# Kernel optimization log

Hardware: AMD Instinct MI355X
Metric: run time of the kernel (lower is better)

Reference implementation:

```python
import jax, jax.numpy as jnp
import numpy as np

B = 2048
LATENT = 32
FRAME = 256
COND = 1
HIDDEN = 256
FUT = 1
E = 8
GATE_H = 64
IN_SIZE = LATENT + FRAME * COND      # 288
INTER = LATENT + HIDDEN              # 288 (must equal IN_SIZE, see forward)
OUT_SIZE = FUT * FRAME               # 256


def setup_inputs() -> dict:
    key = jax.random.key(0)
    ks = jax.random.split(key, 16)

    def kaiming(k, shape, fan_in):
        bound = np.sqrt(6.0 / fan_in).astype(np.float32)
        return jax.random.uniform(k, shape, jnp.float32, -bound, bound)

    z = jax.random.normal(ks[0], (B, IN_SIZE), jnp.float32)
    # gate MLP: Linear(IN_SIZE,64) -> ELU -> Linear(64,64) -> ELU -> Linear(64,E)
    g0_w = kaiming(ks[1], (IN_SIZE, GATE_H), IN_SIZE)
    g0_b = jnp.zeros((GATE_H,), jnp.float32)
    g1_w = kaiming(ks[2], (GATE_H, GATE_H), GATE_H)
    g1_b = jnp.zeros((GATE_H,), jnp.float32)
    g2_w = kaiming(ks[3], (GATE_H, E), GATE_H)
    g2_b = jnp.zeros((E,), jnp.float32)
    # expert layers (kaiming_uniform over [E, in, out]; bias filled with 0.01)
    w0 = kaiming(ks[4], (E, IN_SIZE, HIDDEN), IN_SIZE)
    b0 = jnp.full((E, HIDDEN), 0.01, jnp.float32)
    w1 = kaiming(ks[5], (E, INTER, HIDDEN), INTER)
    b1 = jnp.full((E, HIDDEN), 0.01, jnp.float32)
    w2 = kaiming(ks[6], (E, INTER, OUT_SIZE), INTER)
    b2 = jnp.full((E, OUT_SIZE), 0.01, jnp.float32)
    return dict(z=z, g0_w=g0_w, g0_b=g0_b, g1_w=g1_w, g1_b=g1_b,
                g2_w=g2_w, g2_b=g2_b, w0=w0, b0=b0, w1=w1, b1=b1, w2=w2, b2=b2)


def reference(z, g0_w, g0_b, g1_w, g1_b, g2_w, g2_b, w0, b0, w1, b1, w2, b2):
    # gating network -> softmax coefficients [B, E]
    h = jax.nn.elu(z @ g0_w + g0_b)
    h = jax.nn.elu(h @ g1_w + g1_b)
    coefficients = jax.nn.softmax(h @ g2_w + g2_b, axis=1)

    layers = [(w0, b0, True), (w1, b1, True), (w2, b2, False)]
    layer_out = None
    for weight, bias, has_act in layers:
        # materialize per-sample mixed weights (matches torch.matmul(coef, flat_weight).view(...))
        mixed_weight = jnp.einsum('be,eio->bio', coefficients, weight)  # [B, in, out]
        mixed_bias = coefficients @ bias                                 # [B, out]
        # baddbmm with z as [B,1,in]: per-sample vec-mat product
        out = jnp.einsum('bi,bio->bo', z, mixed_weight) + mixed_bias
        layer_out = jax.nn.elu(out) if has_act else out
    return layer_out
```

## Files before the change

### kernel.cpp

```cpp
#include <hip/hip_runtime.h>
#include <hip/hip_bf16.h>

#define B_TOTAL 2048
#define IN_SZ   288
#define GH      64
#define E_NUM   8
#define OUT_N   256
#define NKT     9

#define W2T_BLKS 576
#define ZF_BLKS  32
#define GWF_BLKS 4
#define GWF_FRAGS 46

typedef __attribute__((ext_vector_type(8))) short bf16x8;
typedef __attribute__((ext_vector_type(4))) float f32x4;

__device__ __forceinline__ float elu_f(float x) {
    return x > 0.0f ? x : (expf(x) - 1.0f);
}
__device__ __forceinline__ ushort f2bf(float f) {
    __hip_bfloat16 h = __float2bfloat16(f);
    return *reinterpret_cast<ushort*>(&h);
}

__global__ __launch_bounds__(256) void prep_kernel(
    const float* __restrict__ w2, const float* __restrict__ z,
    const float* __restrict__ g0_w, const float* __restrict__ g1_w,
    const float* __restrict__ g2_w,
    ushort* __restrict__ w2f, ushort* __restrict__ zf, ushort* __restrict__ gwf)
{
    __shared__ float ts[32][36];
    const int t = threadIdx.x;
    const int wid = t >> 6, l = t & 63;
    const int fr = l & 15, fg = l >> 4;

    if (blockIdx.x < W2T_BLKS) {
        const int e  = blockIdx.x / 72;
        const int r_ = blockIdx.x - e * 72;
        const int kt = r_ >> 3;
        const int og = r_ & 7;
        const int o0 = og * 32;
        const float* src = w2 + ((size_t)e * IN_SZ + kt * 32) * OUT_N + o0;
        {
            int r = t >> 3, c4 = t & 7;
            *(float4*)&ts[r][c4 * 4] = *(const float4*)(src + (size_t)r * OUT_N + c4 * 4);
        }
        __syncthreads();
        {
            const int fl   = t >> 7;
            const int half = (t >> 6) & 1;
            const int ll   = t & 63;
            const int qfr = ll & 15, qfg = ll >> 4;
            const int nt = og * 2 + fl;
            ushort4 u;
            u.x = f2bf(ts[qfg * 8 + half * 4 + 0][fl * 16 + qfr]);
            u.y = f2bf(ts[qfg * 8 + half * 4 + 1][fl * 16 + qfr]);
            u.z = f2bf(ts[qfg * 8 + half * 4 + 2][fl * 16 + qfr]);
            u.w = f2bf(ts[qfg * 8 + half * 4 + 3][fl * 16 + qfr]);
            size_t off = ((size_t)((e * 16 + nt) * NKT + kt)) * 512 + ll * 8 + half * 4;
            *(ushort4*)&w2f[off] = u;
        }
        return;
    }

    if (blockIdx.x < W2T_BLKS + ZF_BLKS) {
        const int mt = (blockIdx.x - W2T_BLKS) * 4 + wid;
        const int m0 = mt * 16;
        const float* zr = z + (size_t)(m0 + fr) * IN_SZ + fg * 8;
        #pragma unroll
        for (int kt = 0; kt < NKT; ++kt) {
            float4 v0 = *(const float4*)(zr + kt * 32);
            float4 v1 = *(const float4*)(zr + kt * 32 + 4);
            ushort4 u0, u1;
            u0.x = f2bf(v0.x); u0.y = f2bf(v0.y); u0.z = f2bf(v0.z); u0.w = f2bf(v0.w);
            u1.x = f2bf(v1.x); u1.y = f2bf(v1.y); u1.z = f2bf(v1.z); u1.w = f2bf(v1.w);
            size_t off = ((size_t)(mt * NKT + kt)) * 512 + l * 8;
            *(ushort4*)&zf[off]     = u0;
            *(ushort4*)&zf[off + 4] = u1;
        }
        return;
    }

    const int base = (blockIdx.x - W2T_BLKS - ZF_BLKS) * 4 + wid;
    for (int fid = base; fid < GWF_FRAGS; fid += 16) {
        float vals[8];
        if (fid < 36) {
            int nt = fid / NKT, kt = fid - nt * NKT;
            #pragma unroll
            for (int j = 0; j < 8; ++j) {
                int k = kt * 32 + fg * 8 + j;
                vals[j] = g0_w[k * GH + nt * 16 + fr];
            }
        } else if (fid < 44) {
            int q = fid - 36, nt = q >> 1, kk = q & 1;
            #pragma unroll
            for (int j = 0; j < 8; ++j) {
                int k = kk * 32 + fg * 8 + j;
                vals[j] = g1_w[k * GH + nt * 16 + fr];
            }
        } else {
            int kk = fid - 44;
            #pragma unroll
            for (int j = 0; j < 8; ++j) {
                int k = kk * 32 + fg * 8 + j;
                vals[j] = (fr < E_NUM) ? g2_w[k * E_NUM + fr] : 0.0f;
            }
        }
        ushort4 u0, u1;
        u0.x = f2bf(vals[0]); u0.y = f2bf(vals[1]); u0.z = f2bf(vals[2]); u0.w = f2bf(vals[3]);
        u1.x = f2bf(vals[4]); u1.y = f2bf(vals[5]); u1.z = f2bf(vals[6]); u1.w = f2bf(vals[7]);
        size_t off = (size_t)fid * 512 + l * 8;
        *(ushort4*)&gwf[off]     = u0;
        *(ushort4*)&gwf[off + 4] = u1;
    }
}

__global__ __launch_bounds__(128) void fused_kernel(
    const ushort* __restrict__ zf, const ushort* __restrict__ w2f,
    const ushort* __restrict__ gwf,
    const float* __restrict__ g0_b, const float* __restrict__ g1_b,
    const float* __restrict__ g2_b, const float* __restrict__ b2,
    float* __restrict__ out)
{
    __shared__ ushort hscr[2][16][72];
    __shared__ float  lgs[2][16][8];
    __shared__ float  cfsT[2][E_NUM][16];

    const int t = threadIdx.x, wv = t >> 6, l = t & 63;
    const int fr = l & 15, fg = l >> 4, fk = fg * 8;
    const int mt = blockIdx.x * 2 + wv, m0 = mt * 16;
    const int nt = blockIdx.y, n0 = nt * 16;

    bf16x8 A[9];
    #pragma unroll
    for (int kt = 0; kt < NKT; ++kt)
        A[kt] = *(const bf16x8*)(zf + ((size_t)(mt * NKT + kt)) * 512 + l * 8);

    #pragma unroll
    for (int ng = 0; ng < 4; ++ng) {
        f32x4 g = {0.f, 0.f, 0.f, 0.f};
        #pragma unroll
        for (int kt = 0; kt < NKT; ++kt) {
            bf16x8 b = *(const bf16x8*)(gwf + ((size_t)(ng * NKT + kt)) * 512 + l * 8);
            g = __builtin_amdgcn_mfma_f32_16x16x32_bf16(A[kt], b, g, 0, 0, 0);
        }
        float bias = g0_b[ng * 16 + fr];
        #pragma unroll
        for (int j = 0; j < 4; ++j)
            hscr[wv][fg * 4 + j][ng * 16 + fr] = f2bf(elu_f(g[j] + bias));
    }
    __syncthreads();

    {
        bf16x8 hA[2];
        #pragma unroll
        for (int kk = 0; kk < 2; ++kk)
            hA[kk] = *(const bf16x8*)&hscr[wv][fr][kk * 32 + fk];
        f32x4 gacc[4];
        #pragma unroll
        for (int ng = 0; ng < 4; ++ng) {
            f32x4 g = {0.f, 0.f, 0.f, 0.f};
            #pragma unroll
            for (int kk = 0; kk < 2; ++kk) {
                bf16x8 b = *(const bf16x8*)(gwf + ((size_t)(36 + ng * 2 + kk)) * 512 + l * 8);
                g = __builtin_amdgcn_mfma_f32_16x16x32_bf16(hA[kk], b, g, 0, 0, 0);
            }
            gacc[ng] = g;
        }
        __syncthreads();
        #pragma unroll
        for (int ng = 0; ng < 4; ++ng) {
            float bias = g1_b[ng * 16 + fr];
            #pragma unroll
            for (int j = 0; j < 4; ++j)
                hscr[wv][fg * 4 + j][ng * 16 + fr] = f2bf(elu_f(gacc[ng][j] + bias));
        }
    }
    __syncthreads();

    {
        bf16x8 hA[2];
        #pragma unroll
        for (int kk = 0; kk < 2; ++kk)
            hA[kk] = *(const bf16x8*)&hscr[wv][fr][kk * 32 + fk];
        f32x4 g = {0.f, 0.f, 0.f, 0.f};
        #pragma unroll
        for (int kk = 0; kk < 2; ++kk) {
            bf16x8 b = *(const bf16x8*)(gwf + ((size_t)(44 + kk)) * 512 + l * 8);
            g = __builtin_amdgcn_mfma_f32_16x16x32_bf16(hA[kk], b, g, 0, 0, 0);
        }
        if (fr < E_NUM) {
            float bias = g2_b[fr];
            #pragma unroll
            for (int j = 0; j < 4; ++j)
                lgs[wv][fg * 4 + j][fr] = g[j] + bias;
        }
    }
    __syncthreads();

    if (l < 16) {
        float m = lgs[wv][l][0];
        #pragma unroll
        for (int k = 1; k < E_NUM; ++k) m = fmaxf(m, lgs[wv][l][k]);
        float s = 0.f;
        float ex[E_NUM];
        #pragma unroll
        for (int k = 0; k < E_NUM; ++k) { ex[k] = expf(lgs[wv][l][k] - m); s += ex[k]; }
        float inv = 1.0f / s;
        #pragma unroll
        for (int k = 0; k < E_NUM; ++k) cfsT[wv][k][l] = ex[k] * inv;
    }
    __syncthreads();

    const ushort* Bp = w2f + (size_t)nt * NKT * 512 + l * 8;

    f32x4 acc = {0.f, 0.f, 0.f, 0.f};
    bf16x8 B[9];
    #pragma unroll
    for (int kt = 0; kt < NKT; ++kt)
        B[kt] = *(const bf16x8*)(Bp + (size_t)kt * 512);

    #pragma unroll
    for (int e = 0; e < E_NUM; ++e) {
        bf16x8 Bn[9];
        if (e < E_NUM - 1) {
            #pragma unroll
            for (int kt = 0; kt < NKT; ++kt)
                Bn[kt] = *(const bf16x8*)(Bp + ((size_t)((e + 1) * 16 * NKT) + kt) * 512);
        }
        f32x4 p0 = {0.f, 0.f, 0.f, 0.f};
        f32x4 p1 = {0.f, 0.f, 0.f, 0.f};
        p0 = __builtin_amdgcn_mfma_f32_16x16x32_bf16(A[0], B[0], p0, 0, 0, 0);
        p1 = __builtin_amdgcn_mfma_f32_16x16x32_bf16(A[1], B[1], p1, 0, 0, 0);
        p0 = __builtin_amdgcn_mfma_f32_16x16x32_bf16(A[2], B[2], p0, 0, 0, 0);
        p1 = __builtin_amdgcn_mfma_f32_16x16x32_bf16(A[3], B[3], p1, 0, 0, 0);
        p0 = __builtin_amdgcn_mfma_f32_16x16x32_bf16(A[4], B[4], p0, 0, 0, 0);
        p1 = __builtin_amdgcn_mfma_f32_16x16x32_bf16(A[5], B[5], p1, 0, 0, 0);
        p0 = __builtin_amdgcn_mfma_f32_16x16x32_bf16(A[6], B[6], p0, 0, 0, 0);
        p1 = __builtin_amdgcn_mfma_f32_16x16x32_bf16(A[7], B[7], p1, 0, 0, 0);
        p0 = __builtin_amdgcn_mfma_f32_16x16x32_bf16(A[8], B[8], p0, 0, 0, 0);

        float4 cv = *(const float4*)&cfsT[wv][e][fg * 4];
        float bv  = b2[e * OUT_N + n0 + fr];
        float ca[4] = {cv.x, cv.y, cv.z, cv.w};
        #pragma unroll
        for (int j = 0; j < 4; ++j)
            acc[j] = fmaf(ca[j], p0[j] + p1[j] + bv, acc[j]);

        #pragma unroll
        for (int kt = 0; kt < NKT; ++kt) B[kt] = Bn[kt];
    }

    #pragma unroll
    for (int j = 0; j < 4; ++j)
        out[(size_t)(m0 + fg * 4 + j) * OUT_N + n0 + fr] = acc[j];
}

__global__ __launch_bounds__(64) void gate_fb_kernel(
    const float* __restrict__ z,
    const float* __restrict__ g0_w, const float* __restrict__ g0_b,
    const float* __restrict__ g1_w, const float* __restrict__ g1_b,
    const float* __restrict__ g2_w, const float* __restrict__ g2_b,
    float* __restrict__ coef)
{
    __shared__ float z_s[IN_SZ];
    __shared__ float h0_s[GH];
    __shared__ float h1_s[GH];
    const int b = blockIdx.x;
    const int t = threadIdx.x;
    const float* zr = z + (size_t)b * IN_SZ;
    for (int i = t; i < IN_SZ; i += 64) z_s[i] = zr[i];
    __syncthreads();
    float a0 = g0_b[t];
    for (int i = 0; i < IN_SZ; ++i) a0 = fmaf(z_s[i], g0_w[i * GH + t], a0);
    h0_s[t] = elu_f(a0);
    __syncthreads();
    float a1 = g1_b[t];
    for (int k = 0; k < GH; ++k) a1 = fmaf(h0_s[k], g1_w[k * GH + t], a1);
    h1_s[t] = elu_f(a1);
    __syncthreads();
    if (t < E_NUM) {
        float lg = g2_b[t];
        for (int k = 0; k < GH; ++k) lg = fmaf(h1_s[k], g2_w[k * E_NUM + t], lg);
        float m = lg;
        for (int d = 1; d < 8; d <<= 1) m = fmaxf(m, __shfl_xor(m, d, 8));
        float ex = expf(lg - m);
        float s = ex;
        for (int d = 1; d < 8; d <<= 1) s += __shfl_xor(s, d, 8);
        coef[b * E_NUM + t] = ex / s;
    }
}

__global__ __launch_bounds__(256) void direct_kernel(
    const float* __restrict__ z, const float* __restrict__ w2,
    const float* __restrict__ b2, const float* __restrict__ coef,
    float* __restrict__ out)
{
    __shared__ float z_s[8][IN_SZ];
    __shared__ float c_s[8][E_NUM];
    const int b0 = blockIdx.x * 8;
    const int t  = threadIdx.x;
    for (int idx = t; idx < 8 * IN_SZ; idx += 256)
        ((float*)z_s)[idx] = z[(size_t)b0 * IN_SZ + idx];
    if (t < 64) c_s[t >> 3][t & 7] = coef[b0 * E_NUM + t];
    __syncthreads();
    float outv[8];
    #pragma unroll
    for (int r = 0; r < 8; ++r) outv[r] = 0.0f;
    for (int e = 0; e < E_NUM; ++e) {
        const float* w = w2 + (size_t)e * IN_SZ * OUT_N + t;
        float tmp[8];
        #pragma unroll
        for (int r = 0; r < 8; ++r) tmp[r] = 0.0f;
        #pragma unroll 4
        for (int i = 0; i < IN_SZ; ++i) {
            float wv = w[i * OUT_N];
            #pragma unroll
            for (int r = 0; r < 8; ++r) tmp[r] += z_s[r][i] * wv;
        }
        float bv = b2[e * OUT_N + t];
        #pragma unroll
        for (int r = 0; r < 8; ++r) outv[r] += c_s[r][e] * (tmp[r] + bv);
    }
    #pragma unroll
    for (int r = 0; r < 8; ++r) out[(size_t)(b0 + r) * OUT_N + t] = outv[r];
}

extern "C" void kernel_launch(void* const* d_in, const int* in_sizes, int n_in,
                              void* d_out, int out_size, void* d_ws, size_t ws_size,
                              hipStream_t stream) {
    const float* z    = (const float*)d_in[0];
    const float* g0_w = (const float*)d_in[1];
    const float* g0_b = (const float*)d_in[2];
    const float* g1_w = (const float*)d_in[3];
    const float* g1_b = (const float*)d_in[4];
    const float* g2_w = (const float*)d_in[5];
    const float* g2_b = (const float*)d_in[6];
    const float* w2   = (const float*)d_in[11];
    const float* b2   = (const float*)d_in[12];
    float* out = (float*)d_out;

    const size_t w2f_b = (size_t)E_NUM * 16 * NKT * 1024;
    const size_t zf_b  = (size_t)128 * NKT * 1024;
    const size_t gwf_b = (size_t)GWF_FRAGS * 1024;

    char* p = (char*)d_ws;
    ushort* w2f = (ushort*)p;            p += w2f_b;
    ushort* zf  = (ushort*)p;            p += zf_b;
    ushort* gwf = (ushort*)p;

    if (ws_size >= w2f_b + zf_b + gwf_b) {
        prep_kernel<<<W2T_BLKS + ZF_BLKS + GWF_BLKS, 256, 0, stream>>>(
            w2, z, g0_w, g1_w, g2_w, w2f, zf, gwf);
        fused_kernel<<<dim3(B_TOTAL / 32, OUT_N / 16), 128, 0, stream>>>(
            zf, w2f, gwf, g0_b, g1_b, g2_b, b2, out);
    } else {
        float* coef = (float*)d_ws;
        gate_fb_kernel<<<B_TOTAL, 64, 0, stream>>>(z, g0_w, g0_b, g1_w, g1_b,
                                                   g2_w, g2_b, coef);
        direct_kernel<<<B_TOTAL / 8, 256, 0, stream>>>(z, w2, b2, coef, out);
    }
}
```

Measured before the change: 22.91 us.

## Share expert weight tiles across four waves via double-buffered LDS staging

Blocks grow from 2 to 4 waves (64 rows each), and the per-expert w2 fragments are loaded cooperatively into a double-buffered LDS tile, two experts at a time, instead of each wave streaming its own copy from global memory. Register prefetch of the next expert pair overlaps the global loads with the MFMA work. This cuts redundant global/L2 traffic for weights, at the cost of extra LDS use, block-wide barriers, and half as many blocks in the grid.

```diff
diff --git a/kernel.cpp b/kernel.cpp
--- a/kernel.cpp
+++ b/kernel.cpp
@@ -116,26 +116,39 @@
     }
 }
 
-__global__ __launch_bounds__(128) void fused_kernel(
+__global__ __launch_bounds__(256) void fused_kernel(
     const ushort* __restrict__ zf, const ushort* __restrict__ w2f,
     const ushort* __restrict__ gwf,
     const float* __restrict__ g0_b, const float* __restrict__ g1_b,
     const float* __restrict__ g2_b, const float* __restrict__ b2,
     float* __restrict__ out)
 {
-    __shared__ ushort hscr[2][16][72];
-    __shared__ float  lgs[2][16][8];
-    __shared__ float  cfsT[2][E_NUM][16];
+    __shared__ ushort Bl[2][18 * 512];
+    __shared__ ushort hscr[4][16][72];
+    __shared__ float  lgs[4][16][8];
+    __shared__ float  cfsT[4][E_NUM][16];
 
     const int t = threadIdx.x, wv = t >> 6, l = t & 63;
     const int fr = l & 15, fg = l >> 4, fk = fg * 8;
-    const int mt = blockIdx.x * 2 + wv, m0 = mt * 16;
+    const int mt = blockIdx.x * 4 + wv, m0 = mt * 16;
     const int nt = blockIdx.y, n0 = nt * 16;
 
     bf16x8 A[9];
     #pragma unroll
     for (int kt = 0; kt < NKT; ++kt)
         A[kt] = *(const bf16x8*)(zf + ((size_t)(mt * NKT + kt)) * 512 + l * 8);
+
+    const int4* w2f_i4 = (const int4*)w2f;
+    int4 st[5];
+    #pragma unroll
+    for (int it = 0; it < 5; ++it) {
+        int s = t + it * 256;
+        if (s < 1152) {
+            int f = s >> 6, ll = s & 63;
+            int el = (f >= 9) ? 1 : 0, ktf = f - 9 * el;
+            st[it] = w2f_i4[((size_t)((el * 16 + nt) * NKT + ktf)) * 64 + ll];
+        }
+    }
 
     #pragma unroll
     for (int ng = 0; ng < 4; ++ng) {
@@ -213,43 +226,49 @@
     }
     __syncthreads();
 
-    const ushort* Bp = w2f + (size_t)nt * NKT * 512 + l * 8;
-
     f32x4 acc = {0.f, 0.f, 0.f, 0.f};
-    bf16x8 B[9];
-    #pragma unroll
-    for (int kt = 0; kt < NKT; ++kt)
-        B[kt] = *(const bf16x8*)(Bp + (size_t)kt * 512);
-
-    #pragma unroll
-    for (int e = 0; e < E_NUM; ++e) {
-        bf16x8 Bn[9];
-        if (e < E_NUM - 1) {
-            #pragma unroll
-            for (int kt = 0; kt < NKT; ++kt)
-                Bn[kt] = *(const bf16x8*)(Bp + ((size_t)((e + 1) * 16 * NKT) + kt) * 512);
-        }
-        f32x4 p0 = {0.f, 0.f, 0.f, 0.f};
-        f32x4 p1 = {0.f, 0.f, 0.f, 0.f};
-        p0 = __builtin_amdgcn_mfma_f32_16x16x32_bf16(A[0], B[0], p0, 0, 0, 0);
-        p1 = __builtin_amdgcn_mfma_f32_16x16x32_bf16(A[1], B[1], p1, 0, 0, 0);
-        p0 = __builtin_amdgcn_mfma_f32_16x16x32_bf16(A[2], B[2], p0, 0, 0, 0);
-        p1 = __builtin_amdgcn_mfma_f32_16x16x32_bf16(A[3], B[3], p1, 0, 0, 0);
-        p0 = __builtin_amdgcn_mfma_f32_16x16x32_bf16(A[4], B[4], p0, 0, 0, 0);
-        p1 = __builtin_amdgcn_mfma_f32_16x16x32_bf16(A[5], B[5], p1, 0, 0, 0);
-        p0 = __builtin_amdgcn_mfma_f32_16x16x32_bf16(A[6], B[6], p0, 0, 0, 0);
-        p1 = __builtin_amdgcn_mfma_f32_16x16x32_bf16(A[7], B[7], p1, 0, 0, 0);
-        p0 = __builtin_amdgcn_mfma_f32_16x16x32_bf16(A[8], B[8], p0, 0, 0, 0);
-
-        float4 cv = *(const float4*)&cfsT[wv][e][fg * 4];
-        float bv  = b2[e * OUT_N + n0 + fr];
-        float ca[4] = {cv.x, cv.y, cv.z, cv.w};
-        #pragma unroll
-        for (int j = 0; j < 4; ++j)
-            acc[j] = fmaf(ca[j], p0[j] + p1[j] + bv, acc[j]);
-
-        #pragma unroll
-        for (int kt = 0; kt < NKT; ++kt) B[kt] = Bn[kt];
+
+    #pragma unroll
+    for (int ep = 0; ep < 4; ++ep) {
+        const int buf = ep & 1;
+        #pragma unroll
+        for (int it = 0; it < 5; ++it) {
+            int s = t + it * 256;
+            if (s < 1152) ((int4*)&Bl[buf][0])[s] = st[it];
+        }
+        __syncthreads();
+        if (ep < 3) {
+            #pragma unroll
+            for (int it = 0; it < 5; ++it) {
+                int s = t + it * 256;
+                if (s < 1152) {
+                    int f = s >> 6, ll = s & 63;
+                    int el = (f >= 9) ? 1 : 0, ktf = f - 9 * el;
+                    int e = (ep + 1) * 2 + el;
+                    st[it] = w2f_i4[((size_t)((e * 16 + nt) * NKT + ktf)) * 64 + ll];
+                }
+            }
+        }
+        #pragma unroll
+        for (int el = 0; el < 2; ++el) {
+            const int e = ep * 2 + el;
+            const ushort* bp = &Bl[buf][el * 9 * 512] + l * 8;
+            f32x4 p0 = {0.f, 0.f, 0.f, 0.f};
+            f32x4 p1 = {0.f, 0.f, 0.f, 0.f};
+            #pragma unroll
+            for (int kt = 0; kt < NKT; ++kt) {
+                bf16x8 b = *(const bf16x8*)(bp + kt * 512);
+                if (kt & 1) p1 = __builtin_amdgcn_mfma_f32_16x16x32_bf16(A[kt], b, p1, 0, 0, 0);
+                else        p0 = __builtin_amdgcn_mfma_f32_16x16x32_bf16(A[kt], b, p0, 0, 0, 0);
+            }
+            float4 cv = *(const float4*)&cfsT[wv][e][fg * 4];
+            float bv  = b2[e * OUT_N + n0 + fr];
+            float ca[4] = {cv.x, cv.y, cv.z, cv.w};
+            #pragma unroll
+            for (int j = 0; j < 4; ++j)
+                acc[j] = fmaf(ca[j], p0[j] + p1[j] + bv, acc[j]);
+        }
+        __syncthreads();
     }
 
     #pragma unroll
@@ -353,7 +372,7 @@
     if (ws_size >= w2f_b + zf_b + gwf_b) {
         prep_kernel<<<W2T_BLKS + ZF_BLKS + GWF_BLKS, 256, 0, stream>>>(
             w2, z, g0_w, g1_w, g2_w, w2f, zf, gwf);
-        fused_kernel<<<dim3(B_TOTAL / 32, OUT_N / 16), 128, 0, stream>>>(
+        fused_kernel<<<dim3(B_TOTAL / 64, OUT_N / 16), 256, 0, stream>>>(
             zf, w2f, gwf, g0_b, g1_b, g2_b, b2, out);
     } else {
         float* coef = (float*)d_ws;
```

After: 31.57 us. 37.8% more time.

## Share gate MLP across four output-tile waves per row tile

Applied to the files above, without the earlier changes.

Restructures the fused kernel so each 256-thread block handles one 16-row tile and four 16-column output tiles, one per wave. The gate MLP layers are split across the four waves, each computing 16 of the 64 hidden units, and the results are shared through LDS. Before, every block of 128 threads recomputed the full gate network for its rows at each column tile, so the gating work was duplicated 16 times per row. The change cuts that duplication to 4 times, at the cost of more barriers and one wave doing the final logits alone.

```diff
diff --git a/kernel.cpp b/kernel.cpp
--- a/kernel.cpp
+++ b/kernel.cpp
@@ -116,39 +116,38 @@
     }
 }
 
-__global__ __launch_bounds__(128) void fused_kernel(
+__global__ __launch_bounds__(256) void fused_kernel(
     const ushort* __restrict__ zf, const ushort* __restrict__ w2f,
     const ushort* __restrict__ gwf,
     const float* __restrict__ g0_b, const float* __restrict__ g1_b,
     const float* __restrict__ g2_b, const float* __restrict__ b2,
     float* __restrict__ out)
 {
-    __shared__ ushort hscr[2][16][72];
-    __shared__ float  lgs[2][16][8];
-    __shared__ float  cfsT[2][E_NUM][16];
+    __shared__ ushort hscr[16][72];
+    __shared__ float  lgs[16][8];
+    __shared__ float  cfsT[E_NUM][16];
 
     const int t = threadIdx.x, wv = t >> 6, l = t & 63;
     const int fr = l & 15, fg = l >> 4, fk = fg * 8;
-    const int mt = blockIdx.x * 2 + wv, m0 = mt * 16;
-    const int nt = blockIdx.y, n0 = nt * 16;
+    const int mt = blockIdx.x, m0 = mt * 16;
+    const int nt = blockIdx.y * 4 + wv, n0 = nt * 16;
 
     bf16x8 A[9];
     #pragma unroll
     for (int kt = 0; kt < NKT; ++kt)
         A[kt] = *(const bf16x8*)(zf + ((size_t)(mt * NKT + kt)) * 512 + l * 8);
 
-    #pragma unroll
-    for (int ng = 0; ng < 4; ++ng) {
+    {
         f32x4 g = {0.f, 0.f, 0.f, 0.f};
         #pragma unroll
         for (int kt = 0; kt < NKT; ++kt) {
-            bf16x8 b = *(const bf16x8*)(gwf + ((size_t)(ng * NKT + kt)) * 512 + l * 8);
+            bf16x8 b = *(const bf16x8*)(gwf + ((size_t)(wv * NKT + kt)) * 512 + l * 8);
             g = __builtin_amdgcn_mfma_f32_16x16x32_bf16(A[kt], b, g, 0, 0, 0);
         }
-        float bias = g0_b[ng * 16 + fr];
+        float bias = g0_b[wv * 16 + fr];
         #pragma unroll
         for (int j = 0; j < 4; ++j)
-            hscr[wv][fg * 4 + j][ng * 16 + fr] = f2bf(elu_f(g[j] + bias));
+            hscr[fg * 4 + j][wv * 16 + fr] = f2bf(elu_f(g[j] + bias));
     }
     __syncthreads();
 
@@ -156,34 +155,26 @@
         bf16x8 hA[2];
         #pragma unroll
         for (int kk = 0; kk < 2; ++kk)
-            hA[kk] = *(const bf16x8*)&hscr[wv][fr][kk * 32 + fk];
-        f32x4 gacc[4];
-        #pragma unroll
-        for (int ng = 0; ng < 4; ++ng) {
-            f32x4 g = {0.f, 0.f, 0.f, 0.f};
-            #pragma unroll
-            for (int kk = 0; kk < 2; ++kk) {
-                bf16x8 b = *(const bf16x8*)(gwf + ((size_t)(36 + ng * 2 + kk)) * 512 + l * 8);
-                g = __builtin_amdgcn_mfma_f32_16x16x32_bf16(hA[kk], b, g, 0, 0, 0);
-            }
-            gacc[ng] = g;
+            hA[kk] = *(const bf16x8*)&hscr[fr][kk * 32 + fk];
+        f32x4 g = {0.f, 0.f, 0.f, 0.f};
+        #pragma unroll
+        for (int kk = 0; kk < 2; ++kk) {
+            bf16x8 b = *(const bf16x8*)(gwf + ((size_t)(36 + wv * 2 + kk)) * 512 + l * 8);
+            g = __builtin_amdgcn_mfma_f32_16x16x32_bf16(hA[kk], b, g, 0, 0, 0);
         }
         __syncthreads();
-        #pragma unroll
-        for (int ng = 0; ng < 4; ++ng) {
-            float bias = g1_b[ng * 16 + fr];
-            #pragma unroll
-            for (int j = 0; j < 4; ++j)
-                hscr[wv][fg * 4 + j][ng * 16 + fr] = f2bf(elu_f(gacc[ng][j] + bias));
-        }
-    }
-    __syncthreads();
-
-    {
+        float bias = g1_b[wv * 16 + fr];
+        #pragma unroll
+        for (int j = 0; j < 4; ++j)
+            hscr[fg * 4 + j][wv * 16 + fr] = f2bf(elu_f(g[j] + bias));
+    }
+    __syncthreads();
+
+    if (wv == 0) {
         bf16x8 hA[2];
         #pragma unroll
         for (int kk = 0; kk < 2; ++kk)
-            hA[kk] = *(const bf16x8*)&hscr[wv][fr][kk * 32 + fk];
+            hA[kk] = *(const bf16x8*)&hscr[fr][kk * 32 + fk];
         f32x4 g = {0.f, 0.f, 0.f, 0.f};
         #pragma unroll
         for (int kk = 0; kk < 2; ++kk) {
@@ -194,22 +185,22 @@
             float bias = g2_b[fr];
             #pragma unroll
             for (int j = 0; j < 4; ++j)
-                lgs[wv][fg * 4 + j][fr] = g[j] + bias;
-        }
-    }
-    __syncthreads();
-
-    if (l < 16) {
-        float m = lgs[wv][l][0];
-        #pragma unroll
-        for (int k = 1; k < E_NUM; ++k) m = fmaxf(m, lgs[wv][l][k]);
+                lgs[fg * 4 + j][fr] = g[j] + bias;
+        }
+    }
+    __syncthreads();
+
+    if (t < 16) {
+        float m = lgs[t][0];
+        #pragma unroll
+        for (int k = 1; k < E_NUM; ++k) m = fmaxf(m, lgs[t][k]);
         float s = 0.f;
         float ex[E_NUM];
         #pragma unroll
-        for (int k = 0; k < E_NUM; ++k) { ex[k] = expf(lgs[wv][l][k] - m); s += ex[k]; }
+        for (int k = 0; k < E_NUM; ++k) { ex[k] = expf(lgs[t][k] - m); s += ex[k]; }
         float inv = 1.0f / s;
         #pragma unroll
-        for (int k = 0; k < E_NUM; ++k) cfsT[wv][k][l] = ex[k] * inv;
+        for (int k = 0; k < E_NUM; ++k) cfsT[k][t] = ex[k] * inv;
     }
     __syncthreads();
 
@@ -241,7 +232,7 @@
         p1 = __builtin_amdgcn_mfma_f32_16x16x32_bf16(A[7], B[7], p1, 0, 0, 0);
         p0 = __builtin_amdgcn_mfma_f32_16x16x32_bf16(A[8], B[8], p0, 0, 0, 0);
 
-        float4 cv = *(const float4*)&cfsT[wv][e][fg * 4];
+        float4 cv = *(const float4*)&cfsT[e][fg * 4];
         float bv  = b2[e * OUT_N + n0 + fr];
         float ca[4] = {cv.x, cv.y, cv.z, cv.w};
         #pragma unroll
@@ -353,7 +344,7 @@
     if (ws_size >= w2f_b + zf_b + gwf_b) {
         prep_kernel<<<W2T_BLKS + ZF_BLKS + GWF_BLKS, 256, 0, stream>>>(
             w2, z, g0_w, g1_w, g2_w, w2f, zf, gwf);
-        fused_kernel<<<dim3(B_TOTAL / 32, OUT_N / 16), 128, 0, stream>>>(
+        fused_kernel<<<dim3(B_TOTAL / 16, OUT_N / 64), 256, 0, stream>>>(
             zf, w2f, gwf, g0_b, g1_b, g2_b, b2, out);
     } else {
         float* coef = (float*)d_ws;
```

After: 21.08 us. -8.0%, faster.

## Prefetch expert weights before gating, drop block barriers, use 4-wave blocks

Applied to the files above, without the earlier changes.

Moves the first expert's weight fragment loads and all bias loads ahead of the gating MLP so their latency overlaps the gate MFMAs. It removes every __syncthreads, since each wave only touches its own shared-memory slice. It replaces the register copy of the next expert's weights with a ping-pong pair of buffers. Blocks grow from 2 to 4 waves, halving the block count. The cost is higher register pressure from the extra live buffers, and the LDS exchange within a wave now has no explicit barrier or fence.

```diff
diff --git a/kernel.cpp b/kernel.cpp
--- a/kernel.cpp
+++ b/kernel.cpp
@@ -116,26 +116,36 @@
     }
 }
 
-__global__ __launch_bounds__(128) void fused_kernel(
+__global__ __launch_bounds__(256) void fused_kernel(
     const ushort* __restrict__ zf, const ushort* __restrict__ w2f,
     const ushort* __restrict__ gwf,
     const float* __restrict__ g0_b, const float* __restrict__ g1_b,
     const float* __restrict__ g2_b, const float* __restrict__ b2,
     float* __restrict__ out)
 {
-    __shared__ ushort hscr[2][16][72];
-    __shared__ float  lgs[2][16][8];
-    __shared__ float  cfsT[2][E_NUM][16];
+    __shared__ ushort hscr[4][16][72];
+    __shared__ float  lgs[4][16][8];
+    __shared__ float  cfsT[4][E_NUM][16];
 
     const int t = threadIdx.x, wv = t >> 6, l = t & 63;
     const int fr = l & 15, fg = l >> 4, fk = fg * 8;
-    const int mt = blockIdx.x * 2 + wv, m0 = mt * 16;
+    const int mt = blockIdx.x * 4 + wv, m0 = mt * 16;
     const int nt = blockIdx.y, n0 = nt * 16;
 
     bf16x8 A[9];
     #pragma unroll
     for (int kt = 0; kt < NKT; ++kt)
         A[kt] = *(const bf16x8*)(zf + ((size_t)(mt * NKT + kt)) * 512 + l * 8);
+
+    const ushort* Bp = w2f + (size_t)nt * NKT * 512 + l * 8;
+    bf16x8 Bb0[9], Bb1[9];
+    #pragma unroll
+    for (int kt = 0; kt < NKT; ++kt)
+        Bb0[kt] = *(const bf16x8*)(Bp + (size_t)kt * 512);
+    float bvv[E_NUM];
+    #pragma unroll
+    for (int e = 0; e < E_NUM; ++e)
+        bvv[e] = b2[e * OUT_N + n0 + fr];
 
     #pragma unroll
     for (int ng = 0; ng < 4; ++ng) {
@@ -150,7 +160,6 @@
         for (int j = 0; j < 4; ++j)
             hscr[wv][fg * 4 + j][ng * 16 + fr] = f2bf(elu_f(g[j] + bias));
     }
-    __syncthreads();
 
     {
         bf16x8 hA[2];
@@ -168,7 +177,6 @@
             }
             gacc[ng] = g;
         }
-        __syncthreads();
         #pragma unroll
         for (int ng = 0; ng < 4; ++ng) {
             float bias = g1_b[ng * 16 + fr];
@@ -177,7 +185,6 @@
                 hscr[wv][fg * 4 + j][ng * 16 + fr] = f2bf(elu_f(gacc[ng][j] + bias));
         }
     }
-    __syncthreads();
 
     {
         bf16x8 hA[2];
@@ -197,7 +204,6 @@
                 lgs[wv][fg * 4 + j][fr] = g[j] + bias;
         }
     }
-    __syncthreads();
 
     if (l < 16) {
         float m = lgs[wv][l][0];
@@ -211,45 +217,31 @@
         #pragma unroll
         for (int k = 0; k < E_NUM; ++k) cfsT[wv][k][l] = ex[k] * inv;
     }
-    __syncthreads();
-
-    const ushort* Bp = w2f + (size_t)nt * NKT * 512 + l * 8;
 
     f32x4 acc = {0.f, 0.f, 0.f, 0.f};
-    bf16x8 B[9];
-    #pragma unroll
-    for (int kt = 0; kt < NKT; ++kt)
-        B[kt] = *(const bf16x8*)(Bp + (size_t)kt * 512);
 
     #pragma unroll
     for (int e = 0; e < E_NUM; ++e) {
-        bf16x8 Bn[9];
         if (e < E_NUM - 1) {
             #pragma unroll
-            for (int kt = 0; kt < NKT; ++kt)
-                Bn[kt] = *(const bf16x8*)(Bp + ((size_t)((e + 1) * 16 * NKT) + kt) * 512);
+            for (int kt = 0; kt < NKT; ++kt) {
+                bf16x8 v = *(const bf16x8*)(Bp + ((size_t)((e + 1) * 16 * NKT) + kt) * 512);
+                if (e & 1) Bb0[kt] = v; else Bb1[kt] = v;
+            }
         }
         f32x4 p0 = {0.f, 0.f, 0.f, 0.f};
         f32x4 p1 = {0.f, 0.f, 0.f, 0.f};
-        p0 = __builtin_amdgcn_mfma_f32_16x16x32_bf16(A[0], B[0], p0, 0, 0, 0);
-        p1 = __builtin_amdgcn_mfma_f32_16x16x32_bf16(A[1], B[1], p1, 0, 0, 0);
-        p0 = __builtin_amdgcn_mfma_f32_16x16x32_bf16(A[2], B[2], p0, 0, 0, 0);
-        p1 = __builtin_amdgcn_mfma_f32_16x16x32_bf16(A[3], B[3], p1, 0, 0, 0);
-        p0 = __builtin_amdgcn_mfma_f32_16x16x32_bf16(A[4], B[4], p0, 0, 0, 0);
-        p1 = __builtin_amdgcn_mfma_f32_16x16x32_bf16(A[5], B[5], p1, 0, 0, 0);
-        p0 = __builtin_amdgcn_mfma_f32_16x16x32_bf16(A[6], B[6], p0, 0, 0, 0);
-        p1 = __builtin_amdgcn_mfma_f32_16x16x32_bf16(A[7], B[7], p1, 0, 0, 0);
-        p0 = __builtin_amdgcn_mfma_f32_16x16x32_bf16(A[8], B[8], p0, 0, 0, 0);
-
+        #pragma unroll
+        for (int kt = 0; kt < NKT; ++kt) {
+            bf16x8 b = (e & 1) ? Bb1[kt] : Bb0[kt];
+            if (kt & 1) p1 = __builtin_amdgcn_mfma_f32_16x16x32_bf16(A[kt], b, p1, 0, 0, 0);
+            else        p0 = __builtin_amdgcn_mfma_f32_16x16x32_bf16(A[kt], b, p0, 0, 0, 0);
+        }
         float4 cv = *(const float4*)&cfsT[wv][e][fg * 4];
-        float bv  = b2[e * OUT_N + n0 + fr];
         float ca[4] = {cv.x, cv.y, cv.z, cv.w};
         #pragma unroll
         for (int j = 0; j < 4; ++j)
-            acc[j] = fmaf(ca[j], p0[j] + p1[j] + bv, acc[j]);
-
-        #pragma unroll
-        for (int kt = 0; kt < NKT; ++kt) B[kt] = Bn[kt];
+            acc[j] = fmaf(ca[j], p0[j] + p1[j] + bvv[e], acc[j]);
     }
 
     #pragma unroll
@@ -353,7 +345,7 @@
     if (ws_size >= w2f_b + zf_b + gwf_b) {
         prep_kernel<<<W2T_BLKS + ZF_BLKS + GWF_BLKS, 256, 0, stream>>>(
             w2, z, g0_w, g1_w, g2_w, w2f, zf, gwf);
-        fused_kernel<<<dim3(B_TOTAL / 32, OUT_N / 16), 128, 0, stream>>>(
+        fused_kernel<<<dim3(128 / 4, OUT_N / 16), 256, 0, stream>>>(
             zf, w2f, gwf, g0_b, g1_b, g2_b, b2, out);
     } else {
         float* coef = (float*)d_ws;
```

Result: faster. 21.70 us (-5.3%).
